# Performance work log

Hardware: AMD Instinct MI355X
Metric: run time of the kernel (lower is better)

## Reference

```python
import jax, jax.numpy as jnp
import numpy as np
import math

D_MODEL = 512
NHEAD = 8
D_HEAD = D_MODEL // NHEAD
CUT_IDX = 1024
ALPHA = 0.02
BETA = 0.5
B, N = 4, 2048


def setup_inputs() -> dict:
    key = jax.random.key(0)
    ks = jax.random.split(key, 16)
    s = 1.0 / math.sqrt(D_MODEL)
    inp = {
        "x": jax.random.normal(ks[0], (B, N, D_MODEL), dtype=jnp.float32),
        "key_padding_mask": jnp.zeros((B, N), dtype=bool),
        "Wq": jax.random.uniform(ks[1], (D_MODEL, D_MODEL), minval=-s, maxval=s),
        "bq": jax.random.uniform(ks[2], (D_MODEL,), minval=-s, maxval=s),
        "Wk": jax.random.uniform(ks[3], (D_MODEL, D_MODEL), minval=-s, maxval=s),
        "bk": jax.random.uniform(ks[4], (D_MODEL,), minval=-s, maxval=s),
        "Wv": jax.random.uniform(ks[5], (D_MODEL, D_MODEL), minval=-s, maxval=s),
        "bv": jax.random.uniform(ks[6], (D_MODEL,), minval=-s, maxval=s),
        "Wo": jax.random.uniform(ks[7], (D_MODEL, D_MODEL), minval=-s, maxval=s),
        "bo": jax.random.uniform(ks[8], (D_MODEL,), minval=-s, maxval=s),
    }
    return inp


def reference(x, key_padding_mask, Wq, bq, Wk, bk, Wv, bv, Wo, bo):
    Bx, Nx, D = x.shape
    H, Dh = NHEAD, D_HEAD
    # projections (torch Linear: y = x @ W.T + b), split into heads -> (B,H,N,Dh)
    q = (x @ Wq.T + bq).reshape(Bx, Nx, H, Dh).transpose(0, 2, 1, 3)
    k = (x @ Wk.T + bk).reshape(Bx, Nx, H, Dh).transpose(0, 2, 1, 3)
    v = (x @ Wv.T + bv).reshape(Bx, Nx, H, Dh).transpose(0, 2, 1, 3)
    logits = jnp.einsum("bhqd,bhkd->bhqk", q, k) / math.sqrt(Dh)
    idx = jnp.arange(Nx, dtype=jnp.float32)
    dist = jnp.abs(idx[None, :] - idx[:, None])  # (N,N)
    logits = logits - max(ALPHA, 0.0) * dist[None, None, :, :]
    # cut-site bias: depends only on key index j
    cut_bias = jnp.abs(idx - float(CUT_IDX))  # (N,)
    logits = logits - max(BETA, 0.0) * cut_bias[None, None, None, :]
    mask = key_padding_mask[:, None, None, :]
    logits = jnp.where(mask, -jnp.inf, logits)
    attn = jax.nn.softmax(logits, axis=-1)  # (B,H,N,N); dropout is identity (p=0 / eval)
    out = jnp.einsum("bhqk,bhkd->bhqd", attn, v)
    out = out.transpose(0, 2, 1, 3).reshape(Bx, Nx, D)
    out = out @ Wo.T + bo
    return (out, attn)
```

## Files before the change

kernel.cpp:

```cpp
#include <hip/hip_runtime.h>
#include <hip/hip_bf16.h>

typedef __attribute__((ext_vector_type(8))) short bf16x8;
typedef __attribute__((ext_vector_type(4))) float f32x4;
typedef unsigned short u16;

#define DEV static __device__ __forceinline__

#define W0 976
#define WN 96

DEV u16 f2bf(float f) {
  union { float f; unsigned u; } v; v.f = f;
  return (u16)((v.u + 0x7FFFu + ((v.u >> 16) & 1u)) >> 16);
}

DEV float exp2a(float x) {
  float r;
  asm("v_exp_f32 %0, %1" : "=v"(r) : "v"(x));
  return r;
}

DEV void zero_chunk(float* __restrict__ attn, int chunk) {
  const f32x4 z = {0.f, 0.f, 0.f, 0.f};
  f32x4* p = (f32x4*)attn + (size_t)chunk * 16384 + threadIdx.x;
#pragma unroll
  for (int j = 0; j < 64; ++j)
    __builtin_nontemporal_store(z, p + j * 256);
}

DEV void zero_skip(float* __restrict__ base, int row0, int nrows, int tcount) {
  const f32x4 z = {0.f, 0.f, 0.f, 0.f};
  const int total = nrows * 488;
  for (int idx = threadIdx.x; idx < total; idx += tcount) {
    int row = idx / 488, u = idx - row * 488;
    int col4 = (u < 244) ? u : (u + 24);
    __builtin_nontemporal_store(z, (f32x4*)base + (size_t)(row0 + row) * 512 + col4);
  }
}


__global__ __launch_bounds__(256) void cvt_kernel(
    const float* __restrict__ x, const float* __restrict__ Wq,
    const float* __restrict__ Wk, const float* __restrict__ Wv,
    const float* __restrict__ Wo, const unsigned char* __restrict__ mask,
    u16* __restrict__ xb, u16* __restrict__ Wb, u16* __restrict__ Wob,
    float* __restrict__ cutb, float* __restrict__ attn) {
  if (blockIdx.x >= 5152) { zero_chunk(attn, blockIdx.x - 5152); return; }
  int g = blockIdx.x * 256 + threadIdx.x;
  if (g < 1048576) {
    float4 v = ((const float4*)x)[g];
    ushort4 o;
    o.x = f2bf(v.x); o.y = f2bf(v.y); o.z = f2bf(v.z); o.w = f2bf(v.w);
    ((ushort4*)xb)[g] = o;
  } else if (g < 1310720) {
    int t = g - 1048576;
    int w = t >> 16;
    int off = t & 65535;
    const float* src = (w == 0) ? Wq : (w == 1) ? Wk : (w == 2) ? Wv : Wo;
    u16* dst = (w < 3) ? (Wb + (size_t)w * 262144) : Wob;
    float4 v = ((const float4*)src)[off];
    ushort4 o;
    o.x = f2bf(v.x); o.y = f2bf(v.y); o.z = f2bf(v.z); o.w = f2bf(v.w);
    ((ushort4*)dst)[off] = o;
  } else if (g < 1318912) {
    int t = g - 1310720;
    int key = t & 2047;
    float c = -0.72134752f * fabsf((float)key - 1024.0f);
    if (mask[t]) c = -1e30f;
    cutb[t] = c;
  }
}

__global__ __launch_bounds__(256) void gemm_q(
    const u16* __restrict__ xb, const u16* __restrict__ Wb,
    const float* __restrict__ bq, u16* __restrict__ Qs,
    float* __restrict__ attn) {
  if (blockIdx.x >= 256) { zero_chunk(attn, 320 + blockIdx.x - 256); return; }
  __shared__ __align__(16) u16 As[128 * 32];
  __shared__ __align__(16) u16 Bs[128 * 32];
  const int tid = threadIdx.x, lane = tid & 63, wv = tid >> 6;
  const int fr = lane & 15, fg = lane >> 4;
  const int wr = wv >> 1, wc = wv & 1;
  const int m0 = (blockIdx.x & 63) * 128, n0 = (blockIdx.x >> 6) * 128;
  f32x4 acc[4][4] = {};
  const int c0 = wv * 128;
  for (int kt = 0; kt < 512; kt += 32) {
#pragma unroll
    for (int i = 0; i < 2; ++i) {
      int c = c0 + i * 64 + lane;
      int row = c >> 2, cg = c & 3;
      const u16* ga = xb + (size_t)(m0 + row) * 512 + kt + cg * 8;
      const u16* gb = Wb + (size_t)(n0 + row) * 512 + kt + cg * 8;
      __builtin_amdgcn_global_load_lds(
          (const __attribute__((address_space(1))) void*)ga,
          (__attribute__((address_space(3))) void*)(As + (c0 + i * 64) * 8), 16, 0, 0);
      __builtin_amdgcn_global_load_lds(
          (const __attribute__((address_space(1))) void*)gb,
          (__attribute__((address_space(3))) void*)(Bs + (c0 + i * 64) * 8), 16, 0, 0);
    }
    __syncthreads();
    bf16x8 af[4], bf[4];
#pragma unroll
    for (int mi = 0; mi < 4; ++mi)
      af[mi] = *(const bf16x8*)(As + (wr * 64 + mi * 16 + fr) * 32 + fg * 8);
#pragma unroll
    for (int ni = 0; ni < 4; ++ni)
      bf[ni] = *(const bf16x8*)(Bs + (wc * 64 + ni * 16 + fr) * 32 + fg * 8);
#pragma unroll
    for (int mi = 0; mi < 4; ++mi)
#pragma unroll
      for (int ni = 0; ni < 4; ++ni)
        acc[mi][ni] = __builtin_amdgcn_mfma_f32_16x16x32_bf16(af[mi], bf[ni], acc[mi][ni], 0, 0, 0);
    __syncthreads();
  }
#pragma unroll
  for (int ni = 0; ni < 4; ++ni) {
    int n = n0 + wc * 64 + ni * 16 + fr;
    float bias = bq[n];
#pragma unroll
    for (int mi = 0; mi < 4; ++mi)
#pragma unroll
      for (int r = 0; r < 4; ++r) {
        int m = m0 + wr * 64 + mi * 16 + fg * 4 + r;
        Qs[(size_t)m * 512 + n] = f2bf((acc[mi][ni][r] + bias) * 0.125f);
      }
  }
}

__global__ __launch_bounds__(256) void gemm_kv(
    const u16* __restrict__ xb, const u16* __restrict__ Wb,
    const float* __restrict__ bk, const float* __restrict__ bv,
    u16* __restrict__ Kw, u16* __restrict__ VTw, float* __restrict__ attn) {
  if (blockIdx.x >= 32) { zero_chunk(attn, 896 + blockIdx.x - 32); return; }
  __shared__ __align__(16) u16 As[128 * 32];
  __shared__ __align__(16) u16 Bs[128 * 32];
  const int tid = threadIdx.x, lane = tid & 63, wv = tid >> 6;
  const int fr = lane & 15, fg = lane >> 4;
  const int wr = wv >> 1, wc = wv & 1;
  const int b = blockIdx.x & 3, n0 = (blockIdx.x >> 2) * 128;
  const size_t arow0 = (size_t)b * 2048 + W0;
  f32x4 acc[4][4] = {};
  const int c0 = wv * 128;
  for (int kt = 0; kt < 512; kt += 32) {
#pragma unroll
    for (int i = 0; i < 2; ++i) {
      int c = c0 + i * 64 + lane;
      int row = c >> 2, cg = c & 3;
      const u16* ga = xb + (arow0 + row) * 512 + kt + cg * 8;
      const u16* gb = Wb + (size_t)(512 + n0 + row) * 512 + kt + cg * 8;
      __builtin_amdgcn_global_load_lds(
          (const __attribute__((address_space(1))) void*)ga,
          (__attribute__((address_space(3))) void*)(As + (c0 + i * 64) * 8), 16, 0, 0);
      __builtin_amdgcn_global_load_lds(
          (const __attribute__((address_space(1))) void*)gb,
          (__attribute__((address_space(3))) void*)(Bs + (c0 + i * 64) * 8), 16, 0, 0);
    }
    __syncthreads();
    bf16x8 af[4], bf[4];
#pragma unroll
    for (int mi = 0; mi < 4; ++mi)
      af[mi] = *(const bf16x8*)(As + (wr * 64 + mi * 16 + fr) * 32 + fg * 8);
#pragma unroll
    for (int ni = 0; ni < 4; ++ni)
      bf[ni] = *(const bf16x8*)(Bs + (wc * 64 + ni * 16 + fr) * 32 + fg * 8);
#pragma unroll
    for (int mi = 0; mi < 4; ++mi)
#pragma unroll
      for (int ni = 0; ni < 4; ++ni)
        acc[mi][ni] = __builtin_amdgcn_mfma_f32_16x16x32_bf16(af[mi], bf[ni], acc[mi][ni], 0, 0, 0);
    __syncthreads();
  }
#pragma unroll
  for (int ni = 0; ni < 4; ++ni) {
    int n = n0 + wc * 64 + ni * 16 + fr;
    float bias = (n < 512) ? bk[n] : bv[n - 512];
#pragma unroll
    for (int mi = 0; mi < 4; ++mi)
#pragma unroll
      for (int r = 0; r < 4; ++r) {
        int row = wr * 64 + mi * 16 + fg * 4 + r;
        if (row < WN) {
          u16 val = f2bf(acc[mi][ni][r] + bias);
          if (n < 512) {
            int h = n >> 6, dh = n & 63;
            Kw[((size_t)(b * 8 + h) * WN + row) * 64 + dh] = val;
          } else {
            int g = n - 512, h = g >> 6, dh = g & 63;
            VTw[((size_t)(b * 8 + h) * 64 + dh) * WN + row] = val;
          }
        }
      }
  }
}

__global__ __launch_bounds__(512) void attn_kernel(
    const u16* __restrict__ Qs, const u16* __restrict__ Kw,
    const u16* __restrict__ VTw, const float* __restrict__ cutb,
    float* __restrict__ attn, u16* __restrict__ ctx) {
  __shared__ __align__(16) u16 KL[WN * 64];
  __shared__ __align__(16) u16 VTL[64 * 104];
  __shared__ __align__(16) u16 PL[8][16 * 104];
  __shared__ float CBL[WN];
  const int tid = threadIdx.x, lane = tid & 63, wv = tid >> 6;
  const int fr = lane & 15, fg = lane >> 4;
  const int bid = blockIdx.x;
  const int swz = (bid & 7) * 64 + (bid >> 3);
  const int b = swz >> 7, h = (swz >> 4) & 7, qt = swz & 15;
  const int q0 = qt * 128 + wv * 16;
  const size_t tok0 = (size_t)b * 2048;
  const u16* Kbh = Kw + (size_t)(b * 8 + h) * (WN * 64);
  const u16* Vbh = VTw + (size_t)(b * 8 + h) * (WN * 64);

  for (int i = tid; i < 768; i += 512) {
    int srow = i >> 3, ss = i & 7, sc = ss ^ (srow & 7);
    __builtin_amdgcn_global_load_lds(
        (const __attribute__((address_space(1))) void*)(Kbh + srow * 64 + sc * 8),
        (__attribute__((address_space(3))) void*)(KL + (size_t)(i - lane) * 8), 16, 0, 0);
  }
  bf16x8 vst[2];
  int nst = 0;
  for (int i = tid; i < 768; i += 512)
    vst[nst++] = *(const bf16x8*)(Vbh + (i / 12) * WN + (i % 12) * 8);
  float cbv = 0.f;
  if (tid < WN) cbv = cutb[tok0 + W0 + tid];
  bf16x8 aq[2];
#pragma unroll
  for (int c = 0; c < 2; ++c)
    aq[c] = *(const bf16x8*)(Qs + (tok0 + q0 + fr) * 512 + h * 64 + c * 32 + fg * 8);
  {
    int k = 0;
    for (int i = tid; i < 768; i += 512, ++k)
      *(bf16x8*)&VTL[(i / 12) * 104 + (i % 12) * 8] = vst[k];
  }
  if (tid < WN) CBL[tid] = cbv;
  __syncthreads();

  f32x4 av[6];
#pragma unroll
  for (int kb = 0; kb < 6; ++kb) {
    const int row = kb * 16 + fr;
    const int rx = row & 7;
    bf16x8 k0 = *(const bf16x8*)(KL + row * 64 + ((fg ^ rx) * 8));
    bf16x8 k1 = *(const bf16x8*)(KL + row * 64 + (((4 + fg) ^ rx) * 8));
    f32x4 a = {0.f, 0.f, 0.f, 0.f};
    a = __builtin_amdgcn_mfma_f32_16x16x32_bf16(aq[0], k0, a, 0, 0, 0);
    a = __builtin_amdgcn_mfma_f32_16x16x32_bf16(aq[1], k1, a, 0, 0, 0);
    av[kb] = a;
  }
  const float iif = (float)(q0 + fg * 4);
  float srw[4] = {0.f, 0.f, 0.f, 0.f};
#pragma unroll
  for (int kb = 0; kb < 6; ++kb) {
    const int kw = kb * 16 + fr;
    const float cb = CBL[kw];
    const float dif = iif - (float)(W0 + kw);
#pragma unroll
    for (int r = 0; r < 4; ++r) {
      float t1 = fmaf(-0.0288539008f, fabsf(dif + (float)r), cb);
      float e = exp2a(fmaf(av[kb][r], 1.44269504f, t1));
      av[kb][r] = e;
      srw[r] += e;
    }
  }
#pragma unroll
  for (int d = 1; d < 16; d <<= 1)
#pragma unroll
    for (int i = 0; i < 4; ++i)
      srw[i] += __shfl_xor(srw[i], d, 64);
  float rinv[4];
#pragma unroll
  for (int i = 0; i < 4; ++i) rinv[i] = 1.0f / srw[i];

  float* attn_bh = attn + ((size_t)b * 8 + h) * 2048 * 2048;
#pragma unroll
  for (int kb = 0; kb < 6; ++kb) {
    const int kw = kb * 16 + fr;
#pragma unroll
    for (int r = 0; r < 4; ++r) {
      float P = av[kb][r] * rinv[r];
      __builtin_nontemporal_store(P, attn_bh + (size_t)(q0 + fg * 4 + r) * 2048 + W0 + kw);
      PL[wv][(fg * 4 + r) * 104 + kw] = f2bf(P);
    }
  }
  f32x4 cacc[4] = {};
#pragma unroll
  for (int kc = 0; kc < 3; ++kc) {
    bf16x8 pa = *(const bf16x8*)(PL[wv] + fr * 104 + kc * 32 + fg * 8);
#pragma unroll
    for (int c4 = 0; c4 < 4; ++c4) {
      bf16x8 vf = *(const bf16x8*)(VTL + (c4 * 16 + fr) * 104 + kc * 32 + fg * 8);
      cacc[c4] = __builtin_amdgcn_mfma_f32_16x16x32_bf16(pa, vf, cacc[c4], 0, 0, 0);
    }
  }
#pragma unroll
  for (int c4 = 0; c4 < 4; ++c4)
#pragma unroll
    for (int r = 0; r < 4; ++r) {
      int q = q0 + fg * 4 + r;
      ctx[(tok0 + q) * 512 + h * 64 + c4 * 16 + fr] = f2bf(cacc[c4][r]);
    }

  zero_skip(attn + (size_t)19 * 4194304, bid * 16, 16, 512);
}

__global__ __launch_bounds__(256) void gemm_out(
    const u16* __restrict__ ctx, const u16* __restrict__ Wob,
    const float* __restrict__ bo, float* __restrict__ out,
    float* __restrict__ attn) {
  if (blockIdx.x >= 1024) {
    zero_skip(attn + (size_t)23 * 4194304, (blockIdx.x - 1024) * 32, 32, 256);
    return;
  }
  __shared__ __align__(16) u16 As[64 * 32];
  __shared__ __align__(16) u16 Bs[64 * 32];
  const int tid = threadIdx.x, lane = tid & 63, wv = tid >> 6;
  const int fr = lane & 15, fg = lane >> 4;
  const int wr = wv >> 1, wc = wv & 1;
  const int m0 = (blockIdx.x & 127) * 64, n0 = (blockIdx.x >> 7) * 64;
  f32x4 acc[2][2] = {};
  for (int kt = 0; kt < 512; kt += 32) {
    {
      int row = tid >> 2, cg = tid & 3;
      const u16* ga = ctx + (size_t)(m0 + row) * 512 + kt + cg * 8;
      const u16* gb = Wob + (size_t)(n0 + row) * 512 + kt + cg * 8;
      __builtin_amdgcn_global_load_lds(
          (const __attribute__((address_space(1))) void*)ga,
          (__attribute__((address_space(3))) void*)(As + tid * 8), 16, 0, 0);
      __builtin_amdgcn_global_load_lds(
          (const __attribute__((address_space(1))) void*)gb,
          (__attribute__((address_space(3))) void*)(Bs + tid * 8), 16, 0, 0);
    }
    __syncthreads();
    bf16x8 af[2], bf[2];
#pragma unroll
    for (int mi = 0; mi < 2; ++mi)
      af[mi] = *(const bf16x8*)(As + (wr * 32 + mi * 16 + fr) * 32 + fg * 8);
#pragma unroll
    for (int ni = 0; ni < 2; ++ni)
      bf[ni] = *(const bf16x8*)(Bs + (wc * 32 + ni * 16 + fr) * 32 + fg * 8);
#pragma unroll
    for (int mi = 0; mi < 2; ++mi)
#pragma unroll
      for (int ni = 0; ni < 2; ++ni)
        acc[mi][ni] = __builtin_amdgcn_mfma_f32_16x16x32_bf16(af[mi], bf[ni], acc[mi][ni], 0, 0, 0);
    __syncthreads();
  }
#pragma unroll
  for (int ni = 0; ni < 2; ++ni) {
    int n = n0 + wc * 32 + ni * 16 + fr;
    float bias = bo[n];
#pragma unroll
    for (int mi = 0; mi < 2; ++mi)
#pragma unroll
      for (int r = 0; r < 4; ++r) {
        int m = m0 + wr * 32 + mi * 16 + fg * 4 + r;
        out[(size_t)m * 512 + n] = acc[mi][ni][r] + bias;
      }
  }
}

extern "C" void kernel_launch(void* const* d_in, const int* in_sizes, int n_in,
                              void* d_out, int out_size, void* d_ws, size_t ws_size,
                              hipStream_t stream) {
  const float* x = (const float*)d_in[0];
  const unsigned char* mask = (const unsigned char*)d_in[1];
  const float* Wq = (const float*)d_in[2];
  const float* bq = (const float*)d_in[3];
  const float* Wk = (const float*)d_in[4];
  const float* bk = (const float*)d_in[5];
  const float* Wv = (const float*)d_in[6];
  const float* bv = (const float*)d_in[7];
  const float* Wo = (const float*)d_in[8];
  const float* bo = (const float*)d_in[9];
  float* out = (float*)d_out;
  float* attn = out + (size_t)4 * 2048 * 512;

  char* ws = (char*)d_ws;
  size_t off = 0;
  u16* xb   = (u16*)(ws + off); off += (size_t)8192 * 512 * 2;
  u16* Wb   = (u16*)(ws + off); off += (size_t)1536 * 512 * 2;
  u16* Wob  = (u16*)(ws + off); off += (size_t)512 * 512 * 2;
  u16* Qs   = (u16*)(ws + off); off += (size_t)8192 * 512 * 2;
  u16* Kw   = (u16*)(ws + off); off += (size_t)32 * WN * 64 * 2;
  u16* VTw  = (u16*)(ws + off); off += (size_t)32 * WN * 64 * 2;
  u16* ctx  = (u16*)(ws + off); off += (size_t)8192 * 512 * 2;
  float* cutb = (float*)(ws + off); off += (size_t)8192 * 4;
  if (ws_size < off) return;

  cvt_kernel<<<5472, 256, 0, stream>>>(x, Wq, Wk, Wv, Wo, mask, xb, Wb, Wob, cutb, attn);
  gemm_q<<<832, 256, 0, stream>>>(xb, Wb, bq, Qs, attn);
  gemm_kv<<<352, 256, 0, stream>>>(xb, Wb, bk, bv, Kw, VTw, attn);
  attn_kernel<<<512, 512, 0, stream>>>(Qs, Kw, VTw, cutb, attn, ctx);
  gemm_out<<<1600, 256, 0, stream>>>(ctx, Wob, bo, out, attn);
}
```

Measured before the change: 139.9 us.

## Merge Q and KV projection GEMMs into one launch and rebalance attn zero-fill

New measurement: 134.0 us. 4.2% less time.

```diff
diff --git a/kernel.cpp b/kernel.cpp
--- a/kernel.cpp
+++ b/kernel.cpp
@@ -72,17 +72,31 @@
   }
 }
 
-__global__ __launch_bounds__(256) void gemm_q(
+__global__ __launch_bounds__(256) void gemm_qkv(
     const u16* __restrict__ xb, const u16* __restrict__ Wb,
-    const float* __restrict__ bq, u16* __restrict__ Qs,
-    float* __restrict__ attn) {
-  if (blockIdx.x >= 256) { zero_chunk(attn, 320 + blockIdx.x - 256); return; }
+    const float* __restrict__ bq, const float* __restrict__ bk,
+    const float* __restrict__ bv, u16* __restrict__ Qs,
+    u16* __restrict__ Kw, u16* __restrict__ VTw, float* __restrict__ attn) {
+  if (blockIdx.x >= 288) { zero_chunk(attn, 512 + blockIdx.x - 288); return; }
   __shared__ __align__(16) u16 As[128 * 32];
   __shared__ __align__(16) u16 Bs[128 * 32];
   const int tid = threadIdx.x, lane = tid & 63, wv = tid >> 6;
   const int fr = lane & 15, fg = lane >> 4;
   const int wr = wv >> 1, wc = wv & 1;
-  const int m0 = (blockIdx.x & 63) * 128, n0 = (blockIdx.x >> 6) * 128;
+  const bool isq = blockIdx.x < 256;
+  int m0, n0;
+  size_t abase;
+  if (isq) {
+    m0 = (blockIdx.x & 63) * 128;
+    n0 = (blockIdx.x >> 6) * 128;
+    abase = (size_t)m0 * 512;
+  } else {
+    int kb = blockIdx.x - 256;
+    m0 = 0;
+    n0 = (kb >> 2) * 128;
+    abase = ((size_t)(kb & 3) * 2048 + W0) * 512;
+  }
+  const int brow0 = isq ? 0 : 512;
   f32x4 acc[4][4] = {};
   const int c0 = wv * 128;
   for (int kt = 0; kt < 512; kt += 32) {
@@ -90,8 +104,8 @@
     for (int i = 0; i < 2; ++i) {
       int c = c0 + i * 64 + lane;
       int row = c >> 2, cg = c & 3;
-      const u16* ga = xb + (size_t)(m0 + row) * 512 + kt + cg * 8;
-      const u16* gb = Wb + (size_t)(n0 + row) * 512 + kt + cg * 8;
+      const u16* ga = xb + abase + (size_t)row * 512 + kt + cg * 8;
+      const u16* gb = Wb + (size_t)(brow0 + n0 + row) * 512 + kt + cg * 8;
       __builtin_amdgcn_global_load_lds(
           (const __attribute__((address_space(1))) void*)ga,
           (__attribute__((address_space(3))) void*)(As + (c0 + i * 64) * 8), 16, 0, 0);
@@ -114,83 +128,42 @@
         acc[mi][ni] = __builtin_amdgcn_mfma_f32_16x16x32_bf16(af[mi], bf[ni], acc[mi][ni], 0, 0, 0);
     __syncthreads();
   }
-#pragma unroll
-  for (int ni = 0; ni < 4; ++ni) {
-    int n = n0 + wc * 64 + ni * 16 + fr;
-    float bias = bq[n];
-#pragma unroll
-    for (int mi = 0; mi < 4; ++mi)
-#pragma unroll
-      for (int r = 0; r < 4; ++r) {
-        int m = m0 + wr * 64 + mi * 16 + fg * 4 + r;
-        Qs[(size_t)m * 512 + n] = f2bf((acc[mi][ni][r] + bias) * 0.125f);
-      }
-  }
-}
-
-__global__ __launch_bounds__(256) void gemm_kv(
-    const u16* __restrict__ xb, const u16* __restrict__ Wb,
-    const float* __restrict__ bk, const float* __restrict__ bv,
-    u16* __restrict__ Kw, u16* __restrict__ VTw, float* __restrict__ attn) {
-  if (blockIdx.x >= 32) { zero_chunk(attn, 896 + blockIdx.x - 32); return; }
-  __shared__ __align__(16) u16 As[128 * 32];
-  __shared__ __align__(16) u16 Bs[128 * 32];
-  const int tid = threadIdx.x, lane = tid & 63, wv = tid >> 6;
-  const int fr = lane & 15, fg = lane >> 4;
-  const int wr = wv >> 1, wc = wv & 1;
-  const int b = blockIdx.x & 3, n0 = (blockIdx.x >> 2) * 128;
-  const size_t arow0 = (size_t)b * 2048 + W0;
-  f32x4 acc[4][4] = {};
-  const int c0 = wv * 128;
-  for (int kt = 0; kt < 512; kt += 32) {
-#pragma unroll
-    for (int i = 0; i < 2; ++i) {
-      int c = c0 + i * 64 + lane;
-      int row = c >> 2, cg = c & 3;
-      const u16* ga = xb + (arow0 + row) * 512 + kt + cg * 8;
-      const u16* gb = Wb + (size_t)(512 + n0 + row) * 512 + kt + cg * 8;
-      __builtin_amdgcn_global_load_lds(
-          (const __attribute__((address_space(1))) void*)ga,
-          (__attribute__((address_space(3))) void*)(As + (c0 + i * 64) * 8), 16, 0, 0);
-      __builtin_amdgcn_global_load_lds(
-          (const __attribute__((address_space(1))) void*)gb,
-          (__attribute__((address_space(3))) void*)(Bs + (c0 + i * 64) * 8), 16, 0, 0);
-    }
-    __syncthreads();
-    bf16x8 af[4], bf[4];
-#pragma unroll
-    for (int mi = 0; mi < 4; ++mi)
-      af[mi] = *(const bf16x8*)(As + (wr * 64 + mi * 16 + fr) * 32 + fg * 8);
-#pragma unroll
-    for (int ni = 0; ni < 4; ++ni)
-      bf[ni] = *(const bf16x8*)(Bs + (wc * 64 + ni * 16 + fr) * 32 + fg * 8);
-#pragma unroll
-    for (int mi = 0; mi < 4; ++mi)
-#pragma unroll
-      for (int ni = 0; ni < 4; ++ni)
-        acc[mi][ni] = __builtin_amdgcn_mfma_f32_16x16x32_bf16(af[mi], bf[ni], acc[mi][ni], 0, 0, 0);
-    __syncthreads();
-  }
-#pragma unroll
-  for (int ni = 0; ni < 4; ++ni) {
-    int n = n0 + wc * 64 + ni * 16 + fr;
-    float bias = (n < 512) ? bk[n] : bv[n - 512];
-#pragma unroll
-    for (int mi = 0; mi < 4; ++mi)
-#pragma unroll
-      for (int r = 0; r < 4; ++r) {
-        int row = wr * 64 + mi * 16 + fg * 4 + r;
-        if (row < WN) {
-          u16 val = f2bf(acc[mi][ni][r] + bias);
-          if (n < 512) {
-            int h = n >> 6, dh = n & 63;
-            Kw[((size_t)(b * 8 + h) * WN + row) * 64 + dh] = val;
-          } else {
-            int g = n - 512, h = g >> 6, dh = g & 63;
-            VTw[((size_t)(b * 8 + h) * 64 + dh) * WN + row] = val;
+  if (isq) {
+#pragma unroll
+    for (int ni = 0; ni < 4; ++ni) {
+      int n = n0 + wc * 64 + ni * 16 + fr;
+      float bias = bq[n];
+#pragma unroll
+      for (int mi = 0; mi < 4; ++mi)
+#pragma unroll
+        for (int r = 0; r < 4; ++r) {
+          int m = m0 + wr * 64 + mi * 16 + fg * 4 + r;
+          Qs[(size_t)m * 512 + n] = f2bf((acc[mi][ni][r] + bias) * 0.125f);
+        }
+    }
+  } else {
+    const int b = (blockIdx.x - 256) & 3;
+#pragma unroll
+    for (int ni = 0; ni < 4; ++ni) {
+      int n = n0 + wc * 64 + ni * 16 + fr;
+      float bias = (n < 512) ? bk[n] : bv[n - 512];
+#pragma unroll
+      for (int mi = 0; mi < 4; ++mi)
+#pragma unroll
+        for (int r = 0; r < 4; ++r) {
+          int row = wr * 64 + mi * 16 + fg * 4 + r;
+          if (row < WN) {
+            u16 val = f2bf(acc[mi][ni][r] + bias);
+            if (n < 512) {
+              int h = n >> 6, dh = n & 63;
+              Kw[((size_t)(b * 8 + h) * WN + row) * 64 + dh] = val;
+            } else {
+              int g = n - 512, h = g >> 6, dh = g & 63;
+              VTw[((size_t)(b * 8 + h) * 64 + dh) * WN + row] = val;
+            }
           }
         }
-      }
+    }
   }
 }
 
@@ -300,16 +273,14 @@
       int q = q0 + fg * 4 + r;
       ctx[(tok0 + q) * 512 + h * 64 + c4 * 16 + fr] = f2bf(cacc[c4][r]);
     }
-
-  zero_skip(attn + (size_t)19 * 4194304, bid * 16, 16, 512);
 }
 
 __global__ __launch_bounds__(256) void gemm_out(
     const u16* __restrict__ ctx, const u16* __restrict__ Wob,
     const float* __restrict__ bo, float* __restrict__ out,
     float* __restrict__ attn) {
-  if (blockIdx.x >= 1024) {
-    zero_skip(attn + (size_t)23 * 4194304, (blockIdx.x - 1024) * 32, 32, 256);
+  if (blockIdx.x < 576) {
+    zero_skip(attn + (size_t)23 * 4194304, blockIdx.x * 32, 32, 256);
     return;
   }
   __shared__ __align__(16) u16 As[64 * 32];
@@ -317,7 +288,8 @@
   const int tid = threadIdx.x, lane = tid & 63, wv = tid >> 6;
   const int fr = lane & 15, fg = lane >> 4;
   const int wr = wv >> 1, wc = wv & 1;
-  const int m0 = (blockIdx.x & 127) * 64, n0 = (blockIdx.x >> 7) * 64;
+  const int cb = blockIdx.x - 576;
+  const int m0 = (cb & 127) * 64, n0 = (cb >> 7) * 64;
   f32x4 acc[2][2] = {};
   for (int kt = 0; kt < 512; kt += 32) {
     {
@@ -388,9 +360,8 @@
   float* cutb = (float*)(ws + off); off += (size_t)8192 * 4;
   if (ws_size < off) return;
 
-  cvt_kernel<<<5472, 256, 0, stream>>>(x, Wq, Wk, Wv, Wo, mask, xb, Wb, Wob, cutb, attn);
-  gemm_q<<<832, 256, 0, stream>>>(xb, Wb, bq, Qs, attn);
-  gemm_kv<<<352, 256, 0, stream>>>(xb, Wb, bk, bv, Kw, VTw, attn);
+  cvt_kernel<<<5664, 256, 0, stream>>>(x, Wq, Wk, Wv, Wo, mask, xb, Wb, Wob, cutb, attn);
+  gemm_qkv<<<1248, 256, 0, stream>>>(xb, Wb, bq, bk, bv, Qs, Kw, VTw, attn);
   attn_kernel<<<512, 512, 0, stream>>>(Qs, Kw, VTw, cutb, attn, ctx);
   gemm_out<<<1600, 256, 0, stream>>>(ctx, Wob, bo, out, attn);
 }
```
